# Kernel optimization log

Measured on AMD Instinct MI355X. Metric: run time of the kernel, lower is better.

The kernel has to match this reference:

```python
import jax, jax.numpy as jnp
import numpy as np
import math

B, T, EMB, HEAD = 4, 4096, 768, 64


def setup_inputs() -> dict:
    key = jax.random.key(0)
    kx, kk, kq, kv = jax.random.split(key, 4)
    s = 1.0 / math.sqrt(EMB)  # roughly torch Linear init scale
    return {
        "x": jax.random.normal(kx, (B, T, EMB), dtype=jnp.float32),
        "Wk": jax.random.normal(kk, (EMB, HEAD), dtype=jnp.float32) * s,
        "Wq": jax.random.normal(kq, (EMB, HEAD), dtype=jnp.float32) * s,
        "Wv": jax.random.normal(kv, (EMB, HEAD), dtype=jnp.float32) * s,
    }


def reference(x, Wk, Wq, Wv):
    # x: (B, T, EMB); projections are bias-free Linear layers
    k = x @ Wk  # (B, T, HEAD)
    q = x @ Wq
    v = x @ Wv
    Tcur = x.shape[1]
    scale = 1.0 / math.sqrt(k.shape[-1])
    # (B, Tq, Tk) score matrix, causal masked
    wei = jnp.einsum("bqh,bkh->bqk", q, k) * scale
    causal = jnp.tril(jnp.ones((Tcur, Tcur), dtype=bool))
    wei = jnp.where(causal, wei, -jnp.inf)
    attn = jax.nn.softmax(wei, axis=-1)  # dropout p=0.0 (eval)
    return jnp.einsum("bqk,bkh->bqh", attn, v)  # (B, T, HEAD)
```

## Files before the change

kernel.cpp:

```cpp
#include <hip/hip_runtime.h>
#include <hip/hip_bf16.h>

#define NB 4
#define NT 4096
#define NE 768
#define NH 64

using bf16 = __hip_bfloat16;
typedef __attribute__((ext_vector_type(8))) short bf16x8;
typedef __attribute__((ext_vector_type(4))) float f32x4;
typedef __attribute__((ext_vector_type(16))) float f32x16;
typedef __attribute__((ext_vector_type(4))) unsigned int u32x4;

#define QSCALE 0.18033688011112042f

__device__ inline short f2bfs(float f) {
  bf16 h = __float2bfloat16(f);
  return __builtin_bit_cast(short, h);
}
__device__ inline unsigned pack_bf2(float a, float b) {
  unsigned short ua = __builtin_bit_cast(unsigned short, __float2bfloat16(a));
  unsigned short ub = __builtin_bit_cast(unsigned short, __float2bfloat16(b));
  return ((unsigned)ub << 16) | ua;
}

#define GLOAD_LDS16(gsrc, ldst)                                        \
  __builtin_amdgcn_global_load_lds(                                    \
      (const __attribute__((address_space(1))) void*)(gsrc),           \
      (__attribute__((address_space(3))) void*)(ldst), 16, 0, 0)

__global__ __launch_bounds__(256) void k_wt(const float* __restrict__ Wk,
                                            const float* __restrict__ Wq,
                                            const float* __restrict__ Wv,
                                            bf16* __restrict__ Wt2) {
  __shared__ float xl[32][65];
  const int m = blockIdx.x / 24;
  const int ks = blockIdx.x % 24;
  const int tid = threadIdx.x;
  const float* W = (m == 0) ? Wk : ((m == 1) ? Wq : Wv);
  const float scale = (m == 1) ? QSCALE : 1.0f;
  const int e0 = ks * 32;
#pragma unroll
  for (int i = 0; i < 8; ++i) {
    const int lin = i * 256 + tid;
    xl[lin >> 6][lin & 63] = W[(size_t)(e0 + (lin >> 6)) * NH + (lin & 63)];
  }
  __syncthreads();
  const int lane = tid & 63, w = tid >> 6;
  const int cbg = m * 4 + w;
  bf16x8 t;
#pragma unroll
  for (int j = 0; j < 8; ++j)
    t[j] = f2bfs(xl[((lane >> 4) << 3) + j][w * 16 + (lane & 15)] * scale);
  *reinterpret_cast<bf16x8*>(Wt2 + (((size_t)cbg * 24 + ks) * 64 + lane) * 8) = t;
}

__global__ __launch_bounds__(256) void k_proj(const float* __restrict__ x,
                                              const bf16* __restrict__ Wt2,
                                              bf16* __restrict__ Q,
                                              bf16* __restrict__ K,
                                              bf16* __restrict__ Vt) {
  __shared__ __align__(16) bf16 xl[16][768];
  const int tid = threadIdx.x;
  const int wave = tid >> 6, lane = tid & 63;
  const int lr = lane & 15, lk = lane >> 4;
  const int row0 = blockIdx.x * 16;

#pragma unroll
  for (int j = 0; j < 6; ++j) {
    const int e = (j * 256 + tid) * 8;
    const int row = e / 768;
    const int col = e - row * 768;
    const int chunk = col >> 3;
    const int sch = (chunk & ~7) | ((chunk ^ row) & 7);
    const float* xp = x + (size_t)(row0 + row) * NE + col;
    float4 a0 = *reinterpret_cast<const float4*>(xp);
    float4 a1 = *reinterpret_cast<const float4*>(xp + 4);
    bf16x8 af;
    af[0] = f2bfs(a0.x); af[1] = f2bfs(a0.y); af[2] = f2bfs(a0.z); af[3] = f2bfs(a0.w);
    af[4] = f2bfs(a1.x); af[5] = f2bfs(a1.y); af[6] = f2bfs(a1.z); af[7] = f2bfs(a1.w);
    *reinterpret_cast<bf16x8*>((char*)xl + row * 1536 + sch * 16) = af;
  }
  __syncthreads();

  f32x4 acc[3];
#pragma unroll
  for (int cb = 0; cb < 3; ++cb)
#pragma unroll
    for (int r = 0; r < 4; ++r) acc[cb][r] = 0.f;

#pragma unroll 4
  for (int ks = 0; ks < 24; ++ks) {
    const int chunk = ks * 4 + lk;
    const int sch = (chunk & ~7) | ((chunk ^ lr) & 7);
    bf16x8 af = *reinterpret_cast<const bf16x8*>((const char*)xl + lr * 1536 + sch * 16);
#pragma unroll
    for (int cb = 0; cb < 3; ++cb) {
      bf16x8 bfr = *reinterpret_cast<const bf16x8*>(
          Wt2 + (((size_t)(wave * 3 + cb) * 24 + ks) * 64 + lane) * 8);
      acc[cb] = __builtin_amdgcn_mfma_f32_16x16x32_bf16(af, bfr, acc[cb], 0, 0, 0);
    }
  }

  const int trow = row0 + lk * 4;
#pragma unroll
  for (int cb = 0; cb < 3; ++cb) {
    const int hh0 = (wave * 3 + cb) * 16;
    const int m = hh0 >> 6;
    const int h = (hh0 & 63) + lr;
    if (m == 0) {
#pragma unroll
      for (int r = 0; r < 4; ++r)
        K[(size_t)(trow + r) * NH + h] = __float2bfloat16(acc[cb][r]);
    } else if (m == 1) {
#pragma unroll
      for (int r = 0; r < 4; ++r)
        Q[(size_t)(trow + r) * NH + h] = __float2bfloat16(acc[cb][r]);
    } else {
      const int bb = trow >> 12;
      const int t = trow & (NT - 1);
      ushort4 pk;
      pk.x = (unsigned short)f2bfs(acc[cb][0]);
      pk.y = (unsigned short)f2bfs(acc[cb][1]);
      pk.z = (unsigned short)f2bfs(acc[cb][2]);
      pk.w = (unsigned short)f2bfs(acc[cb][3]);
      *reinterpret_cast<ushort4*>(Vt + (size_t)(bb * NH + h) * NT + t) = pk;
    }
  }
}

__device__ inline void stage_kv(const bf16* Kb, const bf16* Vb, int k0,
                                bf16* Kl, bf16* Vl, int wave, int lane) {
  const int rsub = lane >> 3, ch = lane & 7;
#pragma unroll
  for (int j = 0; j < 2; ++j) {
    const int br = j * 32 + wave * 8;
    const int row = br + rsub;
    const int sch = ch ^ (row & 7);
    GLOAD_LDS16(Kb + (size_t)(k0 + row) * NH + sch * 8, Kl + br * 64);
    GLOAD_LDS16(Vb + (size_t)row * NT + k0 + sch * 8, Vl + br * 64);
  }
}

__global__ __launch_bounds__(256) void k_attn_part(const bf16* __restrict__ Q,
                                                   const bf16* __restrict__ K,
                                                   const bf16* __restrict__ Vt,
                                                   float* __restrict__ part_o,
                                                   float* __restrict__ part_ml,
                                                   int CH, int MAXC) {
  __shared__ __align__(16) bf16 Kl[2][64][64];
  __shared__ __align__(16) bf16 Vl[2][64][64];
  const int tid = threadIdx.x;
  const int wave = tid >> 6, lane = tid & 63;
  const int l31 = lane & 31, hi5 = lane >> 5;
  const int gid = blockIdx.x;
  const int c = gid % MAXC;
  const int srs = (gid / MAXC) & 31;
  const int b = gid / (MAXC * 32);
  const int s = 31 - srs;
  const int ntiles = 2 * s + 2;
  const int nch = (ntiles + CH - 1) / CH;
  if (c >= nch) return;
  const int kt0 = c * CH;
  const int kt1 = min(kt0 + CH, ntiles);
  const int qblk = s * 128;
  const int qrow = 8 * wave + (l31 & 7) + 32 * (l31 >> 3);
  const int qcol = qblk + qrow;

  const bf16* Qb = Q + (size_t)(b * NT + qcol) * NH;
  const bf16* Kb = K + (size_t)b * NT * NH;
  const bf16* Vb = Vt + (size_t)b * NH * NT;

  bf16x8 qf[4];
#pragma unroll
  for (int ks = 0; ks < 4; ++ks)
    qf[ks] = *reinterpret_cast<const bf16x8*>(Qb + ks * 16 + hi5 * 8);

  f32x16 o[2];
#pragma unroll
  for (int hb = 0; hb < 2; ++hb)
#pragma unroll
    for (int r = 0; r < 16; ++r) o[hb][r] = 0.f;
  float m = -1e30f, lsum = 0.f;

  stage_kv(Kb, Vb, kt0 * 64, &Kl[0][0][0], &Vl[0][0][0], wave, lane);

  for (int kt = kt0; kt < kt1; ++kt) {
    const int buf = (kt - kt0) & 1;
    __syncthreads();
    if (kt + 1 < kt1)
      stage_kv(Kb, Vb, (kt + 1) * 64, &Kl[buf ^ 1][0][0], &Vl[buf ^ 1][0][0], wave, lane);
    const int k0 = kt * 64;
    const bf16* Klb = &Kl[buf][0][0];
    const bf16* Vlb = &Vl[buf][0][0];

    f32x16 sa[2];
#pragma unroll
    for (int kb = 0; kb < 2; ++kb) {
#pragma unroll
      for (int r = 0; r < 16; ++r) sa[kb][r] = 0.f;
      __builtin_amdgcn_s_setprio(1);
#pragma unroll
      for (int ks = 0; ks < 4; ++ks) {
        const int row = l31 + 32 * kb;
        const int sch = (hi5 + 2 * ks) ^ (row & 7);
        bf16x8 kf = *reinterpret_cast<const bf16x8*>(Klb + row * 64 + sch * 8);
        sa[kb] = __builtin_amdgcn_mfma_f32_32x32x16_bf16(kf, qf[ks], sa[kb], 0, 0, 0);
      }
      __builtin_amdgcn_s_setprio(0);
    }
    if (kt >= 2 * s) {
#pragma unroll
      for (int kb = 0; kb < 2; ++kb)
#pragma unroll
        for (int r = 0; r < 16; ++r) {
          const int kg = k0 + (r & 3) + 8 * (r >> 2) + 4 * hi5 + 32 * kb;
          if (kg > qcol) sa[kb][r] = -1e30f;
        }
    }
    float pm = sa[0][0];
#pragma unroll
    for (int r = 1; r < 16; ++r) pm = fmaxf(pm, sa[0][r]);
#pragma unroll
    for (int r = 0; r < 16; ++r) pm = fmaxf(pm, sa[1][r]);
    pm = fmaxf(pm, __shfl_xor(pm, 32));
    if (!__all(pm - m <= 6.f)) {
      const float mn = fmaxf(m, pm);
      const float alpha = exp2f(m - mn);
      lsum *= alpha;
#pragma unroll
      for (int hb = 0; hb < 2; ++hb)
#pragma unroll
        for (int r = 0; r < 16; ++r) o[hb][r] *= alpha;
      m = mn;
    }
    float rs = 0.f;
#pragma unroll
    for (int kb = 0; kb < 2; ++kb)
#pragma unroll
      for (int r = 0; r < 16; ++r) {
        const float p = exp2f(sa[kb][r] - m);
        sa[kb][r] = p;
        rs += p;
      }
    rs += __shfl_xor(rs, 32);
    lsum += rs;
    unsigned pk[2][4][2];
#pragma unroll
    for (int kb = 0; kb < 2; ++kb)
#pragma unroll
      for (int q4 = 0; q4 < 4; ++q4)
#pragma unroll
        for (int p = 0; p < 2; ++p)
          pk[kb][q4][p] = pack_bf2(sa[kb][4 * q4 + 2 * p], sa[kb][4 * q4 + 2 * p + 1]);
#pragma unroll
    for (int kb16 = 0; kb16 < 4; ++kb16) {
      const int kb32 = kb16 >> 1;
      const int q4a = 2 * (kb16 & 1);
      const unsigned X0 = pk[kb32][q4a][0], X1 = pk[kb32][q4a][1];
      const unsigned Y0 = pk[kb32][q4a + 1][0], Y1 = pk[kb32][q4a + 1][1];
      const unsigned pX0 = __shfl_xor((int)X0, 32), pX1 = __shfl_xor((int)X1, 32);
      const unsigned pY0 = __shfl_xor((int)Y0, 32), pY1 = __shfl_xor((int)Y1, 32);
      u32x4 pw;
      pw[0] = hi5 ? pY0 : X0;
      pw[1] = hi5 ? pY1 : X1;
      pw[2] = hi5 ? Y0 : pX0;
      pw[3] = hi5 ? Y1 : pX1;
      const bf16x8 pf = __builtin_bit_cast(bf16x8, pw);
      __builtin_amdgcn_s_setprio(1);
#pragma unroll
      for (int hb = 0; hb < 2; ++hb) {
        const int row = l31 + 32 * hb;
        const int sch = (hi5 + 2 * kb16) ^ (row & 7);
        bf16x8 vf = *reinterpret_cast<const bf16x8*>(Vlb + row * 64 + sch * 8);
        o[hb] = __builtin_amdgcn_mfma_f32_32x32x16_bf16(vf, pf, o[hb], 0, 0, 0);
      }
      __builtin_amdgcn_s_setprio(0);
    }
  }

  const size_t idx = (size_t)(b * 32 + s) * MAXC + c;
  float* po = part_o + idx * (128 * 64);
#pragma unroll
  for (int hb = 0; hb < 2; ++hb)
#pragma unroll
    for (int q4 = 0; q4 < 4; ++q4) {
      const int h0 = 32 * hb + 8 * q4 + 4 * hi5;
      float4 v;
      v.x = o[hb][4 * q4 + 0];
      v.y = o[hb][4 * q4 + 1];
      v.z = o[hb][4 * q4 + 2];
      v.w = o[hb][4 * q4 + 3];
      *reinterpret_cast<float4*>(po + (size_t)qrow * 64 + h0) = v;
    }
  if (hi5 == 0) {
    float* pml = part_ml + idx * 256;
    pml[qrow] = m;
    pml[128 + qrow] = lsum;
  }
}

__global__ __launch_bounds__(256) void k_attn_comb(const float* __restrict__ part_o,
                                                   const float* __restrict__ part_ml,
                                                   float* __restrict__ out,
                                                   int CH, int MAXC) {
  const int gid = blockIdx.x;
  const int s = gid & 31;
  const int b = gid >> 5;
  const int row = threadIdx.x >> 1;
  const int half = threadIdx.x & 1;
  const int ntiles = 2 * s + 2;
  const int nc = (ntiles + CH - 1) / CH;
  const size_t base = (size_t)(b * 32 + s) * MAXC;

  float M = -1e30f;
  for (int c = 0; c < nc; ++c)
    M = fmaxf(M, part_ml[(base + c) * 256 + row]);
  float L = 0.f;
  float4 a[8];
#pragma unroll
  for (int k = 0; k < 8; ++k) a[k] = float4{0, 0, 0, 0};
  for (int c = 0; c < nc; ++c) {
    const float mc = part_ml[(base + c) * 256 + row];
    const float lc = part_ml[(base + c) * 256 + 128 + row];
    const float sc = exp2f(mc - M);
    L += lc * sc;
    const float4* op = reinterpret_cast<const float4*>(
        part_o + (base + c) * (128 * 64) + (size_t)row * 64 + half * 32);
#pragma unroll
    for (int k = 0; k < 8; ++k) {
      const float4 v = op[k];
      a[k].x += v.x * sc; a[k].y += v.y * sc;
      a[k].z += v.z * sc; a[k].w += v.w * sc;
    }
  }
  const float inv = 1.f / L;
  float4* outp = reinterpret_cast<float4*>(
      out + (size_t)(b * NT + s * 128 + row) * NH + half * 32);
#pragma unroll
  for (int k = 0; k < 8; ++k) {
    a[k].x *= inv; a[k].y *= inv; a[k].z *= inv; a[k].w *= inv;
    outp[k] = a[k];
  }
}

extern "C" void kernel_launch(void* const* d_in, const int* in_sizes, int n_in,
                              void* d_out, int out_size, void* d_ws, size_t ws_size,
                              hipStream_t stream) {
  const float* x  = (const float*)d_in[0];
  const float* Wk = (const float*)d_in[1];
  const float* Wq = (const float*)d_in[2];
  const float* Wv = (const float*)d_in[3];
  float* out = (float*)d_out;

  char* ws = (char*)d_ws;
  const size_t sz_wt  = (size_t)3 * NH * NE * sizeof(bf16);
  const size_t sz_qkv = (size_t)NB * NT * NH * sizeof(bf16);
  const size_t off_q  = (sz_wt + 255) & ~size_t(255);
  const size_t off_k  = off_q + sz_qkv;
  const size_t off_vt = off_k + sz_qkv;
  const size_t off_pp = off_vt + sz_qkv;

  const size_t per_chunk = (size_t)(128 * 64 + 256) * sizeof(float);
  int CH = 64, MAXC = 1;
  const int opts_ch[3]   = {6, 8, 16};
  const int opts_maxc[3] = {11, 8, 4};
  for (int i = 0; i < 3; ++i) {
    const size_t need = off_pp + (size_t)NB * 32 * opts_maxc[i] * per_chunk;
    if (ws_size >= need) { CH = opts_ch[i]; MAXC = opts_maxc[i]; break; }
  }
  const size_t n_idx = (size_t)NB * 32 * MAXC;
  const size_t off_po = off_pp;
  const size_t off_ml = off_po + n_idx * (128 * 64) * sizeof(float);

  bf16* Wt2 = (bf16*)(ws);
  bf16* Qw  = (bf16*)(ws + off_q);
  bf16* Kw  = (bf16*)(ws + off_k);
  bf16* Vtw = (bf16*)(ws + off_vt);
  float* part_o  = (float*)(ws + off_po);
  float* part_ml = (float*)(ws + off_ml);

  hipLaunchKernelGGL(k_wt, dim3(3 * 24), dim3(256), 0, stream, Wk, Wq, Wv, Wt2);
  hipLaunchKernelGGL(k_proj, dim3(NB * NT / 16), dim3(256), 0, stream,
                     x, Wt2, Qw, Kw, Vtw);
  hipLaunchKernelGGL(k_attn_part, dim3(NB * 32 * MAXC), dim3(256), 0, stream,
                     Qw, Kw, Vtw, part_o, part_ml, CH, MAXC);
  hipLaunchKernelGGL(k_attn_comb, dim3(NB * 32), dim3(256), 0, stream,
                     part_o, part_ml, out, CH, MAXC);
}
```

Measured before the change: 157.3 us.

## Restructure attention into per-wave query blocks and split x conversion out

Attention now gives each wave its own 32-query unit and reads K/V fragments straight from global memory into registers, dropping the LDS double buffer and block-wide syncs. Partial outputs are stored as bf16 and the combine kernel is re-indexed to match the smaller query blocks. x is converted to bf16 in a separate prep kernel fused with the weight transpose. The projection kernel keeps weight fragments in registers and uses a grid split by Q/K/V. This trades extra global traffic and register pressure for finer load balance and no LDS synchronisation, and lowers the precision of the partial outputs.

```diff
diff --git a/kernel.cpp b/kernel.cpp
--- a/kernel.cpp
+++ b/kernel.cpp
@@ -18,6 +18,10 @@
   bf16 h = __float2bfloat16(f);
   return __builtin_bit_cast(short, h);
 }
+__device__ inline float bfs2f(unsigned short u) {
+  unsigned v = ((unsigned)u) << 16;
+  return __builtin_bit_cast(float, v);
+}
 __device__ inline unsigned pack_bf2(float a, float b) {
   unsigned short ua = __builtin_bit_cast(unsigned short, __float2bfloat16(a));
   unsigned short ub = __builtin_bit_cast(unsigned short, __float2bfloat16(b));
@@ -29,143 +33,135 @@
       (const __attribute__((address_space(1))) void*)(gsrc),           \
       (__attribute__((address_space(3))) void*)(ldst), 16, 0, 0)
 
-__global__ __launch_bounds__(256) void k_wt(const float* __restrict__ Wk,
-                                            const float* __restrict__ Wq,
-                                            const float* __restrict__ Wv,
-                                            bf16* __restrict__ Wt2) {
-  __shared__ float xl[32][65];
-  const int m = blockIdx.x / 24;
-  const int ks = blockIdx.x % 24;
+__global__ __launch_bounds__(256) void k_prep(const float* __restrict__ x,
+                                              const float* __restrict__ Wk,
+                                              const float* __restrict__ Wq,
+                                              const float* __restrict__ Wv,
+                                              bf16* __restrict__ Wt2,
+                                              bf16* __restrict__ xb) {
+  __shared__ float wl[32][65];
   const int tid = threadIdx.x;
-  const float* W = (m == 0) ? Wk : ((m == 1) ? Wq : Wv);
-  const float scale = (m == 1) ? QSCALE : 1.0f;
-  const int e0 = ks * 32;
-#pragma unroll
-  for (int i = 0; i < 8; ++i) {
-    const int lin = i * 256 + tid;
-    xl[lin >> 6][lin & 63] = W[(size_t)(e0 + (lin >> 6)) * NH + (lin & 63)];
-  }
-  __syncthreads();
-  const int lane = tid & 63, w = tid >> 6;
-  const int cbg = m * 4 + w;
-  bf16x8 t;
-#pragma unroll
-  for (int j = 0; j < 8; ++j)
-    t[j] = f2bfs(xl[((lane >> 4) << 3) + j][w * 16 + (lane & 15)] * scale);
-  *reinterpret_cast<bf16x8*>(Wt2 + (((size_t)cbg * 24 + ks) * 64 + lane) * 8) = t;
-}
-
-__global__ __launch_bounds__(256) void k_proj(const float* __restrict__ x,
+  if (blockIdx.x < 72) {
+    const int m = blockIdx.x / 24;
+    const int ks = blockIdx.x % 24;
+    const float* W = (m == 0) ? Wk : ((m == 1) ? Wq : Wv);
+    const float scale = (m == 1) ? QSCALE : 1.0f;
+#pragma unroll
+    for (int i = 0; i < 8; ++i) {
+      const int lin = i * 256 + tid;
+      wl[lin >> 6][lin & 63] = W[(size_t)(ks * 32 + (lin >> 6)) * NH + (lin & 63)];
+    }
+    __syncthreads();
+    const int lane = tid & 63, w = tid >> 6;
+    const int cbg = m * 4 + w;
+    bf16x8 t;
+#pragma unroll
+    for (int j = 0; j < 8; ++j)
+      t[j] = f2bfs(wl[((lane >> 4) << 3) + j][w * 16 + (lane & 15)] * scale);
+    *reinterpret_cast<bf16x8*>(Wt2 + (((size_t)cbg * 24 + ks) * 64 + lane) * 8) = t;
+    return;
+  }
+  const size_t e0 = ((size_t)(blockIdx.x - 72) * 256 + tid) * 8;
+  const int row = (int)(e0 / 768);
+  const int col = (int)(e0 - (size_t)row * 768);
+  const int chunk = col >> 3;
+  const int sch = (chunk & ~7) | ((chunk ^ row) & 7);
+  float4 a0 = *reinterpret_cast<const float4*>(x + e0);
+  float4 a1 = *reinterpret_cast<const float4*>(x + e0 + 4);
+  bf16x8 af;
+  af[0] = f2bfs(a0.x); af[1] = f2bfs(a0.y); af[2] = f2bfs(a0.z); af[3] = f2bfs(a0.w);
+  af[4] = f2bfs(a1.x); af[5] = f2bfs(a1.y); af[6] = f2bfs(a1.z); af[7] = f2bfs(a1.w);
+  *reinterpret_cast<bf16x8*>(xb + (size_t)row * 768 + sch * 8) = af;
+}
+
+__global__ __launch_bounds__(256) void k_proj(const bf16* __restrict__ xb,
                                               const bf16* __restrict__ Wt2,
                                               bf16* __restrict__ Q,
                                               bf16* __restrict__ K,
                                               bf16* __restrict__ Vt) {
-  __shared__ __align__(16) bf16 xl[16][768];
+  __shared__ __align__(16) bf16 xl[32][768];
   const int tid = threadIdx.x;
   const int wave = tid >> 6, lane = tid & 63;
   const int lr = lane & 15, lk = lane >> 4;
-  const int row0 = blockIdx.x * 16;
-
-#pragma unroll
-  for (int j = 0; j < 6; ++j) {
-    const int e = (j * 256 + tid) * 8;
-    const int row = e / 768;
-    const int col = e - row * 768;
-    const int chunk = col >> 3;
-    const int sch = (chunk & ~7) | ((chunk ^ row) & 7);
-    const float* xp = x + (size_t)(row0 + row) * NE + col;
-    float4 a0 = *reinterpret_cast<const float4*>(xp);
-    float4 a1 = *reinterpret_cast<const float4*>(xp + 4);
-    bf16x8 af;
-    af[0] = f2bfs(a0.x); af[1] = f2bfs(a0.y); af[2] = f2bfs(a0.z); af[3] = f2bfs(a0.w);
-    af[4] = f2bfs(a1.x); af[5] = f2bfs(a1.y); af[6] = f2bfs(a1.z); af[7] = f2bfs(a1.w);
-    *reinterpret_cast<bf16x8*>((char*)xl + row * 1536 + sch * 16) = af;
-  }
-  __syncthreads();
-
-  f32x4 acc[3];
-#pragma unroll
-  for (int cb = 0; cb < 3; ++cb)
-#pragma unroll
-    for (int r = 0; r < 4; ++r) acc[cb][r] = 0.f;
-
-#pragma unroll 4
-  for (int ks = 0; ks < 24; ++ks) {
-    const int chunk = ks * 4 + lk;
-    const int sch = (chunk & ~7) | ((chunk ^ lr) & 7);
-    bf16x8 af = *reinterpret_cast<const bf16x8*>((const char*)xl + lr * 1536 + sch * 16);
-#pragma unroll
-    for (int cb = 0; cb < 3; ++cb) {
-      bf16x8 bfr = *reinterpret_cast<const bf16x8*>(
-          Wt2 + (((size_t)(wave * 3 + cb) * 24 + ks) * 64 + lane) * 8);
-      acc[cb] = __builtin_amdgcn_mfma_f32_16x16x32_bf16(af, bfr, acc[cb], 0, 0, 0);
-    }
-  }
-
-  const int trow = row0 + lk * 4;
-#pragma unroll
-  for (int cb = 0; cb < 3; ++cb) {
-    const int hh0 = (wave * 3 + cb) * 16;
-    const int m = hh0 >> 6;
-    const int h = (hh0 & 63) + lr;
-    if (m == 0) {
-#pragma unroll
-      for (int r = 0; r < 4; ++r)
-        K[(size_t)(trow + r) * NH + h] = __float2bfloat16(acc[cb][r]);
-    } else if (m == 1) {
-#pragma unroll
-      for (int r = 0; r < 4; ++r)
-        Q[(size_t)(trow + r) * NH + h] = __float2bfloat16(acc[cb][r]);
-    } else {
-      const int bb = trow >> 12;
-      const int t = trow & (NT - 1);
-      ushort4 pk;
-      pk.x = (unsigned short)f2bfs(acc[cb][0]);
-      pk.y = (unsigned short)f2bfs(acc[cb][1]);
-      pk.z = (unsigned short)f2bfs(acc[cb][2]);
-      pk.w = (unsigned short)f2bfs(acc[cb][3]);
-      *reinterpret_cast<ushort4*>(Vt + (size_t)(bb * NH + h) * NT + t) = pk;
-    }
-  }
-}
-
-__device__ inline void stage_kv(const bf16* Kb, const bf16* Vb, int k0,
-                                bf16* Kl, bf16* Vl, int wave, int lane) {
-  const int rsub = lane >> 3, ch = lane & 7;
-#pragma unroll
-  for (int j = 0; j < 2; ++j) {
-    const int br = j * 32 + wave * 8;
-    const int row = br + rsub;
-    const int sch = ch ^ (row & 7);
-    GLOAD_LDS16(Kb + (size_t)(k0 + row) * NH + sch * 8, Kl + br * 64);
-    GLOAD_LDS16(Vb + (size_t)row * NT + k0 + sch * 8, Vl + br * 64);
+  const int m = blockIdx.y;
+  const int cbg = m * 4 + wave;
+
+  bf16x8 wf[24];
+#pragma unroll
+  for (int ks = 0; ks < 24; ++ks)
+    wf[ks] = *reinterpret_cast<const bf16x8*>(
+        Wt2 + (((size_t)cbg * 24 + ks) * 64 + lane) * 8);
+
+  for (int grp = 0; grp < 2; ++grp) {
+    const int t0 = blockIdx.x * 64 + grp * 32;
+#pragma unroll
+    for (int i = 0; i < 12; ++i)
+      GLOAD_LDS16(xb + (size_t)t0 * 768 + ((size_t)i * 256 + tid) * 8,
+                  (char*)xl + (i * 256 + tid) * 16);
+    __syncthreads();
+
+    f32x4 a0, a1;
+#pragma unroll
+    for (int r = 0; r < 4; ++r) { a0[r] = 0.f; a1[r] = 0.f; }
+#pragma unroll
+    for (int ks = 0; ks < 24; ++ks) {
+      const int chunk = ks * 4 + lk;
+      const int sch = (chunk & ~7) | ((chunk ^ lr) & 7);
+      bf16x8 af0 = *reinterpret_cast<const bf16x8*>((const char*)xl + lr * 1536 + sch * 16);
+      bf16x8 af1 = *reinterpret_cast<const bf16x8*>((const char*)xl + (16 + lr) * 1536 + sch * 16);
+      a0 = __builtin_amdgcn_mfma_f32_16x16x32_bf16(af0, wf[ks], a0, 0, 0, 0);
+      a1 = __builtin_amdgcn_mfma_f32_16x16x32_bf16(af1, wf[ks], a1, 0, 0, 0);
+    }
+
+#pragma unroll
+    for (int sub = 0; sub < 2; ++sub) {
+      const f32x4 a = sub ? a1 : a0;
+      const int trow = t0 + sub * 16 + lk * 4;
+      const int h = wave * 16 + lr;
+      if (m == 0) {
+#pragma unroll
+        for (int r = 0; r < 4; ++r)
+          K[(size_t)(trow + r) * NH + h] = __float2bfloat16(a[r]);
+      } else if (m == 1) {
+#pragma unroll
+        for (int r = 0; r < 4; ++r)
+          Q[(size_t)(trow + r) * NH + h] = __float2bfloat16(a[r]);
+      } else {
+        const int bb = trow >> 12;
+        const int t = trow & (NT - 1);
+        ushort4 pk4;
+        pk4.x = (unsigned short)f2bfs(a[0]);
+        pk4.y = (unsigned short)f2bfs(a[1]);
+        pk4.z = (unsigned short)f2bfs(a[2]);
+        pk4.w = (unsigned short)f2bfs(a[3]);
+        *reinterpret_cast<ushort4*>(Vt + (size_t)(bb * NH + h) * NT + t) = pk4;
+      }
+    }
+    __syncthreads();
   }
 }
 
 __global__ __launch_bounds__(256) void k_attn_part(const bf16* __restrict__ Q,
                                                    const bf16* __restrict__ K,
                                                    const bf16* __restrict__ Vt,
-                                                   float* __restrict__ part_o,
+                                                   bf16* __restrict__ part_o,
                                                    float* __restrict__ part_ml,
                                                    int CH, int MAXC) {
-  __shared__ __align__(16) bf16 Kl[2][64][64];
-  __shared__ __align__(16) bf16 Vl[2][64][64];
   const int tid = threadIdx.x;
   const int wave = tid >> 6, lane = tid & 63;
   const int l31 = lane & 31, hi5 = lane >> 5;
-  const int gid = blockIdx.x;
-  const int c = gid % MAXC;
-  const int srs = (gid / MAXC) & 31;
-  const int b = gid / (MAXC * 32);
-  const int s = 31 - srs;
-  const int ntiles = 2 * s + 2;
+  const int unit = blockIdx.x * 4 + wave;
+  const int c = unit % MAXC;
+  const int srs = (unit / MAXC) & 127;
+  const int b = unit / (MAXC * 128);
+  const int s = 127 - srs;
+  const int ntiles = (s >> 1) + 1;
   const int nch = (ntiles + CH - 1) / CH;
   if (c >= nch) return;
-  const int kt0 = c * CH;
-  const int kt1 = min(kt0 + CH, ntiles);
-  const int qblk = s * 128;
-  const int qrow = 8 * wave + (l31 & 7) + 32 * (l31 >> 3);
-  const int qcol = qblk + qrow;
+  const int kt0c = c * CH;
+  const int ktend = min(kt0c + CH, ntiles);
+  const int qblk = s * 32;
+  const int qcol = qblk + l31;
 
   const bf16* Qb = Q + (size_t)(b * NT + qcol) * NH;
   const bf16* Kb = K + (size_t)b * NT * NH;
@@ -183,16 +179,22 @@
     for (int r = 0; r < 16; ++r) o[hb][r] = 0.f;
   float m = -1e30f, lsum = 0.f;
 
-  stage_kv(Kb, Vb, kt0 * 64, &Kl[0][0][0], &Vl[0][0][0], wave, lane);
-
-  for (int kt = kt0; kt < kt1; ++kt) {
-    const int buf = (kt - kt0) & 1;
-    __syncthreads();
-    if (kt + 1 < kt1)
-      stage_kv(Kb, Vb, (kt + 1) * 64, &Kl[buf ^ 1][0][0], &Vl[buf ^ 1][0][0], wave, lane);
+  for (int kt = kt0c; kt < ktend; ++kt) {
     const int k0 = kt * 64;
-    const bf16* Klb = &Kl[buf][0][0];
-    const bf16* Vlb = &Vl[buf][0][0];
+    bf16x8 kf[2][4];
+#pragma unroll
+    for (int kb = 0; kb < 2; ++kb)
+#pragma unroll
+      for (int ks = 0; ks < 4; ++ks)
+        kf[kb][ks] = *reinterpret_cast<const bf16x8*>(
+            Kb + (size_t)(k0 + 32 * kb + l31) * NH + ks * 16 + hi5 * 8);
+    bf16x8 vf[4][2];
+#pragma unroll
+    for (int kb16 = 0; kb16 < 4; ++kb16)
+#pragma unroll
+      for (int hb = 0; hb < 2; ++hb)
+        vf[kb16][hb] = *reinterpret_cast<const bf16x8*>(
+            Vb + (size_t)(l31 + 32 * hb) * NT + k0 + kb16 * 16 + hi5 * 8);
 
     f32x16 sa[2];
 #pragma unroll
@@ -201,15 +203,11 @@
       for (int r = 0; r < 16; ++r) sa[kb][r] = 0.f;
       __builtin_amdgcn_s_setprio(1);
 #pragma unroll
-      for (int ks = 0; ks < 4; ++ks) {
-        const int row = l31 + 32 * kb;
-        const int sch = (hi5 + 2 * ks) ^ (row & 7);
-        bf16x8 kf = *reinterpret_cast<const bf16x8*>(Klb + row * 64 + sch * 8);
-        sa[kb] = __builtin_amdgcn_mfma_f32_32x32x16_bf16(kf, qf[ks], sa[kb], 0, 0, 0);
-      }
+      for (int ks = 0; ks < 4; ++ks)
+        sa[kb] = __builtin_amdgcn_mfma_f32_32x32x16_bf16(kf[kb][ks], qf[ks], sa[kb], 0, 0, 0);
       __builtin_amdgcn_s_setprio(0);
     }
-    if (kt >= 2 * s) {
+    if (kt == ntiles - 1) {
 #pragma unroll
       for (int kb = 0; kb < 2; ++kb)
 #pragma unroll
@@ -218,11 +216,12 @@
           if (kg > qcol) sa[kb][r] = -1e30f;
         }
     }
-    float pm = sa[0][0];
-#pragma unroll
-    for (int r = 1; r < 16; ++r) pm = fmaxf(pm, sa[0][r]);
-#pragma unroll
-    for (int r = 0; r < 16; ++r) pm = fmaxf(pm, sa[1][r]);
+    float t0[8];
+#pragma unroll
+    for (int r = 0; r < 8; ++r)
+      t0[r] = fmaxf(fmaxf(sa[0][r], sa[0][r + 8]), fmaxf(sa[1][r], sa[1][r + 8]));
+    float pm = fmaxf(fmaxf(fmaxf(t0[0], t0[1]), fmaxf(t0[2], t0[3])),
+                     fmaxf(fmaxf(t0[4], t0[5]), fmaxf(t0[6], t0[7])));
     pm = fmaxf(pm, __shfl_xor(pm, 32));
     if (!__all(pm - m <= 6.f)) {
       const float mn = fmaxf(m, pm);
@@ -234,15 +233,17 @@
         for (int r = 0; r < 16; ++r) o[hb][r] *= alpha;
       m = mn;
     }
-    float rs = 0.f;
+    float rs0 = 0.f, rs1 = 0.f, rs2 = 0.f, rs3 = 0.f;
 #pragma unroll
     for (int kb = 0; kb < 2; ++kb)
 #pragma unroll
-      for (int r = 0; r < 16; ++r) {
-        const float p = exp2f(sa[kb][r] - m);
-        sa[kb][r] = p;
-        rs += p;
+      for (int r = 0; r < 16; r += 4) {
+        sa[kb][r] = exp2f(sa[kb][r] - m); rs0 += sa[kb][r];
+        sa[kb][r + 1] = exp2f(sa[kb][r + 1] - m); rs1 += sa[kb][r + 1];
+        sa[kb][r + 2] = exp2f(sa[kb][r + 2] - m); rs2 += sa[kb][r + 2];
+        sa[kb][r + 3] = exp2f(sa[kb][r + 3] - m); rs3 += sa[kb][r + 3];
       }
+    float rs = (rs0 + rs1) + (rs2 + rs3);
     rs += __shfl_xor(rs, 32);
     lsum += rs;
     unsigned pk[2][4][2];
@@ -269,79 +270,68 @@
       const bf16x8 pf = __builtin_bit_cast(bf16x8, pw);
       __builtin_amdgcn_s_setprio(1);
 #pragma unroll
-      for (int hb = 0; hb < 2; ++hb) {
-        const int row = l31 + 32 * hb;
-        const int sch = (hi5 + 2 * kb16) ^ (row & 7);
-        bf16x8 vf = *reinterpret_cast<const bf16x8*>(Vlb + row * 64 + sch * 8);
-        o[hb] = __builtin_amdgcn_mfma_f32_32x32x16_bf16(vf, pf, o[hb], 0, 0, 0);
-      }
+      for (int hb = 0; hb < 2; ++hb)
+        o[hb] = __builtin_amdgcn_mfma_f32_32x32x16_bf16(vf[kb16][hb], pf, o[hb], 0, 0, 0);
       __builtin_amdgcn_s_setprio(0);
     }
   }
 
-  const size_t idx = (size_t)(b * 32 + s) * MAXC + c;
-  float* po = part_o + idx * (128 * 64);
+  const size_t idx = (size_t)(b * 128 + s) * MAXC + c;
+  bf16* po = part_o + idx * (32 * 64);
 #pragma unroll
   for (int hb = 0; hb < 2; ++hb)
 #pragma unroll
     for (int q4 = 0; q4 < 4; ++q4) {
       const int h0 = 32 * hb + 8 * q4 + 4 * hi5;
-      float4 v;
-      v.x = o[hb][4 * q4 + 0];
-      v.y = o[hb][4 * q4 + 1];
-      v.z = o[hb][4 * q4 + 2];
-      v.w = o[hb][4 * q4 + 3];
-      *reinterpret_cast<float4*>(po + (size_t)qrow * 64 + h0) = v;
+      ushort4 pk4;
+      pk4.x = (unsigned short)f2bfs(o[hb][4 * q4 + 0]);
+      pk4.y = (unsigned short)f2bfs(o[hb][4 * q4 + 1]);
+      pk4.z = (unsigned short)f2bfs(o[hb][4 * q4 + 2]);
+      pk4.w = (unsigned short)f2bfs(o[hb][4 * q4 + 3]);
+      *reinterpret_cast<ushort4*>(po + (size_t)l31 * 64 + h0) = pk4;
     }
   if (hi5 == 0) {
-    float* pml = part_ml + idx * 256;
-    pml[qrow] = m;
-    pml[128 + qrow] = lsum;
-  }
-}
-
-__global__ __launch_bounds__(256) void k_attn_comb(const float* __restrict__ part_o,
+    float* pml = part_ml + idx * 64;
+    pml[l31] = m;
+    pml[32 + l31] = lsum;
+  }
+}
+
+__global__ __launch_bounds__(256) void k_attn_comb(const bf16* __restrict__ part_o,
                                                    const float* __restrict__ part_ml,
                                                    float* __restrict__ out,
                                                    int CH, int MAXC) {
   const int gid = blockIdx.x;
-  const int s = gid & 31;
-  const int b = gid >> 5;
-  const int row = threadIdx.x >> 1;
-  const int half = threadIdx.x & 1;
-  const int ntiles = 2 * s + 2;
+  const int rg = gid & 1;
+  const int s = (gid >> 1) & 127;
+  const int b = gid >> 8;
+  const int row = rg * 16 + (threadIdx.x >> 4);
+  const int cq = threadIdx.x & 15;
+  const int ntiles = (s >> 1) + 1;
   const int nc = (ntiles + CH - 1) / CH;
-  const size_t base = (size_t)(b * 32 + s) * MAXC;
+  const size_t base = (size_t)(b * 128 + s) * MAXC;
 
   float M = -1e30f;
   for (int c = 0; c < nc; ++c)
-    M = fmaxf(M, part_ml[(base + c) * 256 + row]);
-  float L = 0.f;
-  float4 a[8];
-#pragma unroll
-  for (int k = 0; k < 8; ++k) a[k] = float4{0, 0, 0, 0};
+    M = fmaxf(M, part_ml[(base + c) * 64 + row]);
+  float L = 0.f, a0 = 0.f, a1 = 0.f, a2 = 0.f, a3 = 0.f;
   for (int c = 0; c < nc; ++c) {
-    const float mc = part_ml[(base + c) * 256 + row];
-    const float lc = part_ml[(base + c) * 256 + 128 + row];
+    const float mc = part_ml[(base + c) * 64 + row];
+    const float lc = part_ml[(base + c) * 64 + 32 + row];
     const float sc = exp2f(mc - M);
     L += lc * sc;
-    const float4* op = reinterpret_cast<const float4*>(
-        part_o + (base + c) * (128 * 64) + (size_t)row * 64 + half * 32);
-#pragma unroll
-    for (int k = 0; k < 8; ++k) {
-      const float4 v = op[k];
-      a[k].x += v.x * sc; a[k].y += v.y * sc;
-      a[k].z += v.z * sc; a[k].w += v.w * sc;
-    }
+    ushort4 v = *reinterpret_cast<const ushort4*>(
+        part_o + (base + c) * (32 * 64) + (size_t)row * 64 + cq * 4);
+    a0 += bfs2f(v.x) * sc;
+    a1 += bfs2f(v.y) * sc;
+    a2 += bfs2f(v.z) * sc;
+    a3 += bfs2f(v.w) * sc;
   }
   const float inv = 1.f / L;
-  float4* outp = reinterpret_cast<float4*>(
-      out + (size_t)(b * NT + s * 128 + row) * NH + half * 32);
-#pragma unroll
-  for (int k = 0; k < 8; ++k) {
-    a[k].x *= inv; a[k].y *= inv; a[k].z *= inv; a[k].w *= inv;
-    outp[k] = a[k];
-  }
+  float4 ov;
+  ov.x = a0 * inv; ov.y = a1 * inv; ov.z = a2 * inv; ov.w = a3 * inv;
+  *reinterpret_cast<float4*>(
+      out + (size_t)(b * NT + s * 32 + row) * NH + cq * 4) = ov;
 }
 
 extern "C" void kernel_launch(void* const* d_in, const int* in_sizes, int n_in,
@@ -354,37 +344,41 @@
   float* out = (float*)d_out;
 
   char* ws = (char*)d_ws;
-  const size_t sz_wt  = (size_t)3 * NH * NE * sizeof(bf16);
+  const size_t sz_wt  = (size_t)12 * 24 * 64 * 8 * sizeof(bf16);
+  const size_t sz_xb  = (size_t)NB * NT * NE * sizeof(bf16);
   const size_t sz_qkv = (size_t)NB * NT * NH * sizeof(bf16);
-  const size_t off_q  = (sz_wt + 255) & ~size_t(255);
+  const size_t off_xb = (sz_wt + 255) & ~size_t(255);
+  const size_t off_q  = off_xb + sz_xb;
   const size_t off_k  = off_q + sz_qkv;
   const size_t off_vt = off_k + sz_qkv;
   const size_t off_pp = off_vt + sz_qkv;
 
-  const size_t per_chunk = (size_t)(128 * 64 + 256) * sizeof(float);
   int CH = 64, MAXC = 1;
-  const int opts_ch[3]   = {6, 8, 16};
-  const int opts_maxc[3] = {11, 8, 4};
-  for (int i = 0; i < 3; ++i) {
-    const size_t need = off_pp + (size_t)NB * 32 * opts_maxc[i] * per_chunk;
+  const int opts_ch[4]   = {4, 8, 16, 64};
+  const int opts_maxc[4] = {16, 8, 4, 1};
+  for (int i = 0; i < 4; ++i) {
+    const size_t n_idx = (size_t)NB * 128 * opts_maxc[i];
+    const size_t need = off_pp + n_idx * (4096 + 256);
     if (ws_size >= need) { CH = opts_ch[i]; MAXC = opts_maxc[i]; break; }
   }
-  const size_t n_idx = (size_t)NB * 32 * MAXC;
+  const size_t n_idx = (size_t)NB * 128 * MAXC;
   const size_t off_po = off_pp;
-  const size_t off_ml = off_po + n_idx * (128 * 64) * sizeof(float);
+  const size_t off_ml = off_po + n_idx * 4096;
 
   bf16* Wt2 = (bf16*)(ws);
+  bf16* xb  = (bf16*)(ws + off_xb);
   bf16* Qw  = (bf16*)(ws + off_q);
   bf16* Kw  = (bf16*)(ws + off_k);
   bf16* Vtw = (bf16*)(ws + off_vt);
-  float* part_o  = (float*)(ws + off_po);
+  bf16* part_o   = (bf16*)(ws + off_po);
   float* part_ml = (float*)(ws + off_ml);
 
-  hipLaunchKernelGGL(k_wt, dim3(3 * 24), dim3(256), 0, stream, Wk, Wq, Wv, Wt2);
-  hipLaunchKernelGGL(k_proj, dim3(NB * NT / 16), dim3(256), 0, stream,
-                     x, Wt2, Qw, Kw, Vtw);
-  hipLaunchKernelGGL(k_attn_part, dim3(NB * 32 * MAXC), dim3(256), 0, stream,
+  hipLaunchKernelGGL(k_prep, dim3(72 + NB * NT * NE / 2048), dim3(256), 0, stream,
+                     x, Wk, Wq, Wv, Wt2, xb);
+  hipLaunchKernelGGL(k_proj, dim3(NB * NT / 64, 3), dim3(256), 0, stream,
+                     xb, Wt2, Qw, Kw, Vtw);
+  hipLaunchKernelGGL(k_attn_part, dim3(NB * 128 * MAXC / 4), dim3(256), 0, stream,
                      Qw, Kw, Vtw, part_o, part_ml, CH, MAXC);
-  hipLaunchKernelGGL(k_attn_comb, dim3(NB * 32), dim3(256), 0, stream,
+  hipLaunchKernelGGL(k_attn_comb, dim3(NB * 128 * 2), dim3(256), 0, stream,
                      part_o, part_ml, out, CH, MAXC);
 }
```

Measured after the change: 179.0 us. 13.8% more time.

## Store bf16 partials, retile projection, widen combine grid, drop setprio, tree reductions

Applied to the files above, without the earlier changes.

The projection kernel now processes 32 rows per block, so each W fragment loaded from global memory feeds two MFMAs. Attention partial outputs are stored as bf16 with nontemporal stores, which halves partial traffic, and the split-K chunk size drops to 4 tiles when the workspace allows. The combine kernel runs eight times as many blocks, with each thread handling four columns. The setprio hints are removed, and the max and sum reductions are split into independent chains for ILP. Rounding the partials to bf16 costs some precision in the final output.

```diff
diff --git a/kernel.cpp b/kernel.cpp
--- a/kernel.cpp
+++ b/kernel.cpp
@@ -18,10 +18,18 @@
   bf16 h = __float2bfloat16(f);
   return __builtin_bit_cast(short, h);
 }
+__device__ inline float bfs2f(unsigned short u) {
+  unsigned v = ((unsigned)u) << 16;
+  return __builtin_bit_cast(float, v);
+}
 __device__ inline unsigned pack_bf2(float a, float b) {
   unsigned short ua = __builtin_bit_cast(unsigned short, __float2bfloat16(a));
   unsigned short ub = __builtin_bit_cast(unsigned short, __float2bfloat16(b));
   return ((unsigned)ub << 16) | ua;
+}
+__device__ inline void nt_store8(void* p, ushort4 v) {
+  __builtin_nontemporal_store(__builtin_bit_cast(unsigned long long, v),
+                              (unsigned long long*)p);
 }
 
 #define GLOAD_LDS16(gsrc, ldst)                                        \
@@ -60,14 +68,14 @@
                                               bf16* __restrict__ Q,
                                               bf16* __restrict__ K,
                                               bf16* __restrict__ Vt) {
-  __shared__ __align__(16) bf16 xl[16][768];
+  __shared__ __align__(16) bf16 xl[32][768];
   const int tid = threadIdx.x;
   const int wave = tid >> 6, lane = tid & 63;
   const int lr = lane & 15, lk = lane >> 4;
-  const int row0 = blockIdx.x * 16;
-
-#pragma unroll
-  for (int j = 0; j < 6; ++j) {
+  const int row0 = blockIdx.x * 32;
+
+#pragma unroll
+  for (int j = 0; j < 12; ++j) {
     const int e = (j * 256 + tid) * 8;
     const int row = e / 768;
     const int col = e - row * 768;
@@ -83,48 +91,54 @@
   }
   __syncthreads();
 
-  f32x4 acc[3];
+  f32x4 acc0[3], acc1[3];
 #pragma unroll
   for (int cb = 0; cb < 3; ++cb)
 #pragma unroll
-    for (int r = 0; r < 4; ++r) acc[cb][r] = 0.f;
+    for (int r = 0; r < 4; ++r) { acc0[cb][r] = 0.f; acc1[cb][r] = 0.f; }
 
 #pragma unroll 4
   for (int ks = 0; ks < 24; ++ks) {
     const int chunk = ks * 4 + lk;
     const int sch = (chunk & ~7) | ((chunk ^ lr) & 7);
-    bf16x8 af = *reinterpret_cast<const bf16x8*>((const char*)xl + lr * 1536 + sch * 16);
+    bf16x8 af0 = *reinterpret_cast<const bf16x8*>((const char*)xl + lr * 1536 + sch * 16);
+    bf16x8 af1 = *reinterpret_cast<const bf16x8*>((const char*)xl + (16 + lr) * 1536 + sch * 16);
 #pragma unroll
     for (int cb = 0; cb < 3; ++cb) {
       bf16x8 bfr = *reinterpret_cast<const bf16x8*>(
           Wt2 + (((size_t)(wave * 3 + cb) * 24 + ks) * 64 + lane) * 8);
-      acc[cb] = __builtin_amdgcn_mfma_f32_16x16x32_bf16(af, bfr, acc[cb], 0, 0, 0);
-    }
-  }
-
-  const int trow = row0 + lk * 4;
-#pragma unroll
-  for (int cb = 0; cb < 3; ++cb) {
-    const int hh0 = (wave * 3 + cb) * 16;
-    const int m = hh0 >> 6;
-    const int h = (hh0 & 63) + lr;
-    if (m == 0) {
-#pragma unroll
-      for (int r = 0; r < 4; ++r)
-        K[(size_t)(trow + r) * NH + h] = __float2bfloat16(acc[cb][r]);
-    } else if (m == 1) {
-#pragma unroll
-      for (int r = 0; r < 4; ++r)
-        Q[(size_t)(trow + r) * NH + h] = __float2bfloat16(acc[cb][r]);
-    } else {
-      const int bb = trow >> 12;
-      const int t = trow & (NT - 1);
-      ushort4 pk;
-      pk.x = (unsigned short)f2bfs(acc[cb][0]);
-      pk.y = (unsigned short)f2bfs(acc[cb][1]);
-      pk.z = (unsigned short)f2bfs(acc[cb][2]);
-      pk.w = (unsigned short)f2bfs(acc[cb][3]);
-      *reinterpret_cast<ushort4*>(Vt + (size_t)(bb * NH + h) * NT + t) = pk;
+      acc0[cb] = __builtin_amdgcn_mfma_f32_16x16x32_bf16(af0, bfr, acc0[cb], 0, 0, 0);
+      acc1[cb] = __builtin_amdgcn_mfma_f32_16x16x32_bf16(af1, bfr, acc1[cb], 0, 0, 0);
+    }
+  }
+
+#pragma unroll
+  for (int st = 0; st < 2; ++st) {
+    const int trow = row0 + st * 16 + lk * 4;
+#pragma unroll
+    for (int cb = 0; cb < 3; ++cb) {
+      const f32x4 a = st ? acc1[cb] : acc0[cb];
+      const int hh0 = (wave * 3 + cb) * 16;
+      const int m = hh0 >> 6;
+      const int h = (hh0 & 63) + lr;
+      if (m == 0) {
+#pragma unroll
+        for (int r = 0; r < 4; ++r)
+          K[(size_t)(trow + r) * NH + h] = __float2bfloat16(a[r]);
+      } else if (m == 1) {
+#pragma unroll
+        for (int r = 0; r < 4; ++r)
+          Q[(size_t)(trow + r) * NH + h] = __float2bfloat16(a[r]);
+      } else {
+        const int bb = trow >> 12;
+        const int t = trow & (NT - 1);
+        ushort4 pk4;
+        pk4.x = (unsigned short)f2bfs(a[0]);
+        pk4.y = (unsigned short)f2bfs(a[1]);
+        pk4.z = (unsigned short)f2bfs(a[2]);
+        pk4.w = (unsigned short)f2bfs(a[3]);
+        *reinterpret_cast<ushort4*>(Vt + (size_t)(bb * NH + h) * NT + t) = pk4;
+      }
     }
   }
 }
@@ -145,7 +159,7 @@
 __global__ __launch_bounds__(256) void k_attn_part(const bf16* __restrict__ Q,
                                                    const bf16* __restrict__ K,
                                                    const bf16* __restrict__ Vt,
-                                                   float* __restrict__ part_o,
+                                                   bf16* __restrict__ part_o,
                                                    float* __restrict__ part_ml,
                                                    int CH, int MAXC) {
   __shared__ __align__(16) bf16 Kl[2][64][64];
@@ -199,7 +213,6 @@
     for (int kb = 0; kb < 2; ++kb) {
 #pragma unroll
       for (int r = 0; r < 16; ++r) sa[kb][r] = 0.f;
-      __builtin_amdgcn_s_setprio(1);
 #pragma unroll
       for (int ks = 0; ks < 4; ++ks) {
         const int row = l31 + 32 * kb;
@@ -207,7 +220,6 @@
         bf16x8 kf = *reinterpret_cast<const bf16x8*>(Klb + row * 64 + sch * 8);
         sa[kb] = __builtin_amdgcn_mfma_f32_32x32x16_bf16(kf, qf[ks], sa[kb], 0, 0, 0);
       }
-      __builtin_amdgcn_s_setprio(0);
     }
     if (kt >= 2 * s) {
 #pragma unroll
@@ -218,11 +230,12 @@
           if (kg > qcol) sa[kb][r] = -1e30f;
         }
     }
-    float pm = sa[0][0];
-#pragma unroll
-    for (int r = 1; r < 16; ++r) pm = fmaxf(pm, sa[0][r]);
-#pragma unroll
-    for (int r = 0; r < 16; ++r) pm = fmaxf(pm, sa[1][r]);
+    float t0[8];
+#pragma unroll
+    for (int r = 0; r < 8; ++r)
+      t0[r] = fmaxf(fmaxf(sa[0][r], sa[0][r + 8]), fmaxf(sa[1][r], sa[1][r + 8]));
+    float pm = fmaxf(fmaxf(fmaxf(t0[0], t0[1]), fmaxf(t0[2], t0[3])),
+                     fmaxf(fmaxf(t0[4], t0[5]), fmaxf(t0[6], t0[7])));
     pm = fmaxf(pm, __shfl_xor(pm, 32));
     if (!__all(pm - m <= 6.f)) {
       const float mn = fmaxf(m, pm);
@@ -234,15 +247,17 @@
         for (int r = 0; r < 16; ++r) o[hb][r] *= alpha;
       m = mn;
     }
-    float rs = 0.f;
+    float rs0 = 0.f, rs1 = 0.f, rs2 = 0.f, rs3 = 0.f;
 #pragma unroll
     for (int kb = 0; kb < 2; ++kb)
 #pragma unroll
-      for (int r = 0; r < 16; ++r) {
-        const float p = exp2f(sa[kb][r] - m);
-        sa[kb][r] = p;
-        rs += p;
+      for (int r = 0; r < 16; r += 4) {
+        sa[kb][r] = exp2f(sa[kb][r] - m); rs0 += sa[kb][r];
+        sa[kb][r + 1] = exp2f(sa[kb][r + 1] - m); rs1 += sa[kb][r + 1];
+        sa[kb][r + 2] = exp2f(sa[kb][r + 2] - m); rs2 += sa[kb][r + 2];
+        sa[kb][r + 3] = exp2f(sa[kb][r + 3] - m); rs3 += sa[kb][r + 3];
       }
+    float rs = (rs0 + rs1) + (rs2 + rs3);
     rs += __shfl_xor(rs, 32);
     lsum += rs;
     unsigned pk[2][4][2];
@@ -267,7 +282,6 @@
       pw[2] = hi5 ? Y0 : pX0;
       pw[3] = hi5 ? Y1 : pX1;
       const bf16x8 pf = __builtin_bit_cast(bf16x8, pw);
-      __builtin_amdgcn_s_setprio(1);
 #pragma unroll
       for (int hb = 0; hb < 2; ++hb) {
         const int row = l31 + 32 * hb;
@@ -275,23 +289,22 @@
         bf16x8 vf = *reinterpret_cast<const bf16x8*>(Vlb + row * 64 + sch * 8);
         o[hb] = __builtin_amdgcn_mfma_f32_32x32x16_bf16(vf, pf, o[hb], 0, 0, 0);
       }
-      __builtin_amdgcn_s_setprio(0);
     }
   }
 
   const size_t idx = (size_t)(b * 32 + s) * MAXC + c;
-  float* po = part_o + idx * (128 * 64);
+  bf16* po = part_o + idx * (128 * 64);
 #pragma unroll
   for (int hb = 0; hb < 2; ++hb)
 #pragma unroll
     for (int q4 = 0; q4 < 4; ++q4) {
       const int h0 = 32 * hb + 8 * q4 + 4 * hi5;
-      float4 v;
-      v.x = o[hb][4 * q4 + 0];
-      v.y = o[hb][4 * q4 + 1];
-      v.z = o[hb][4 * q4 + 2];
-      v.w = o[hb][4 * q4 + 3];
-      *reinterpret_cast<float4*>(po + (size_t)qrow * 64 + h0) = v;
+      ushort4 pk4;
+      pk4.x = (unsigned short)f2bfs(o[hb][4 * q4 + 0]);
+      pk4.y = (unsigned short)f2bfs(o[hb][4 * q4 + 1]);
+      pk4.z = (unsigned short)f2bfs(o[hb][4 * q4 + 2]);
+      pk4.w = (unsigned short)f2bfs(o[hb][4 * q4 + 3]);
+      nt_store8(po + (size_t)qrow * 64 + h0, pk4);
     }
   if (hi5 == 0) {
     float* pml = part_ml + idx * 256;
@@ -300,15 +313,16 @@
   }
 }
 
-__global__ __launch_bounds__(256) void k_attn_comb(const float* __restrict__ part_o,
+__global__ __launch_bounds__(256) void k_attn_comb(const bf16* __restrict__ part_o,
                                                    const float* __restrict__ part_ml,
                                                    float* __restrict__ out,
                                                    int CH, int MAXC) {
   const int gid = blockIdx.x;
-  const int s = gid & 31;
-  const int b = gid >> 5;
-  const int row = threadIdx.x >> 1;
-  const int half = threadIdx.x & 1;
+  const int rg = gid & 7;
+  const int s = (gid >> 3) & 31;
+  const int b = gid >> 8;
+  const int row = rg * 16 + (threadIdx.x >> 4);
+  const int cq = threadIdx.x & 15;
   const int ntiles = 2 * s + 2;
   const int nc = (ntiles + CH - 1) / CH;
   const size_t base = (size_t)(b * 32 + s) * MAXC;
@@ -316,32 +330,24 @@
   float M = -1e30f;
   for (int c = 0; c < nc; ++c)
     M = fmaxf(M, part_ml[(base + c) * 256 + row]);
-  float L = 0.f;
-  float4 a[8];
-#pragma unroll
-  for (int k = 0; k < 8; ++k) a[k] = float4{0, 0, 0, 0};
+  float L = 0.f, a0 = 0.f, a1 = 0.f, a2 = 0.f, a3 = 0.f;
   for (int c = 0; c < nc; ++c) {
     const float mc = part_ml[(base + c) * 256 + row];
     const float lc = part_ml[(base + c) * 256 + 128 + row];
     const float sc = exp2f(mc - M);
     L += lc * sc;
-    const float4* op = reinterpret_cast<const float4*>(
-        part_o + (base + c) * (128 * 64) + (size_t)row * 64 + half * 32);
-#pragma unroll
-    for (int k = 0; k < 8; ++k) {
-      const float4 v = op[k];
-      a[k].x += v.x * sc; a[k].y += v.y * sc;
-      a[k].z += v.z * sc; a[k].w += v.w * sc;
-    }
+    ushort4 v = *reinterpret_cast<const ushort4*>(
+        part_o + (base + c) * (128 * 64) + (size_t)row * 64 + cq * 4);
+    a0 += bfs2f(v.x) * sc;
+    a1 += bfs2f(v.y) * sc;
+    a2 += bfs2f(v.z) * sc;
+    a3 += bfs2f(v.w) * sc;
   }
   const float inv = 1.f / L;
-  float4* outp = reinterpret_cast<float4*>(
-      out + (size_t)(b * NT + s * 128 + row) * NH + half * 32);
-#pragma unroll
-  for (int k = 0; k < 8; ++k) {
-    a[k].x *= inv; a[k].y *= inv; a[k].z *= inv; a[k].w *= inv;
-    outp[k] = a[k];
-  }
+  float4 ov;
+  ov.x = a0 * inv; ov.y = a1 * inv; ov.z = a2 * inv; ov.w = a3 * inv;
+  *reinterpret_cast<float4*>(
+      out + (size_t)(b * NT + s * 128 + row) * NH + cq * 4) = ov;
 }
 
 extern "C" void kernel_launch(void* const* d_in, const int* in_sizes, int n_in,
@@ -354,37 +360,37 @@
   float* out = (float*)d_out;
 
   char* ws = (char*)d_ws;
-  const size_t sz_wt  = (size_t)3 * NH * NE * sizeof(bf16);
+  const size_t sz_wt  = (size_t)12 * 24 * 64 * 8 * sizeof(bf16);
   const size_t sz_qkv = (size_t)NB * NT * NH * sizeof(bf16);
   const size_t off_q  = (sz_wt + 255) & ~size_t(255);
   const size_t off_k  = off_q + sz_qkv;
   const size_t off_vt = off_k + sz_qkv;
   const size_t off_pp = off_vt + sz_qkv;
 
-  const size_t per_chunk = (size_t)(128 * 64 + 256) * sizeof(float);
+  const size_t per_chunk = (size_t)128 * 64 * sizeof(bf16) + 256 * sizeof(float);
   int CH = 64, MAXC = 1;
-  const int opts_ch[3]   = {6, 8, 16};
-  const int opts_maxc[3] = {11, 8, 4};
-  for (int i = 0; i < 3; ++i) {
+  const int opts_ch[4]   = {4, 6, 8, 16};
+  const int opts_maxc[4] = {16, 11, 8, 4};
+  for (int i = 0; i < 4; ++i) {
     const size_t need = off_pp + (size_t)NB * 32 * opts_maxc[i] * per_chunk;
     if (ws_size >= need) { CH = opts_ch[i]; MAXC = opts_maxc[i]; break; }
   }
   const size_t n_idx = (size_t)NB * 32 * MAXC;
   const size_t off_po = off_pp;
-  const size_t off_ml = off_po + n_idx * (128 * 64) * sizeof(float);
+  const size_t off_ml = off_po + n_idx * (size_t)(128 * 64) * sizeof(bf16);
 
   bf16* Wt2 = (bf16*)(ws);
   bf16* Qw  = (bf16*)(ws + off_q);
   bf16* Kw  = (bf16*)(ws + off_k);
   bf16* Vtw = (bf16*)(ws + off_vt);
-  float* part_o  = (float*)(ws + off_po);
+  bf16* part_o   = (bf16*)(ws + off_po);
   float* part_ml = (float*)(ws + off_ml);
 
   hipLaunchKernelGGL(k_wt, dim3(3 * 24), dim3(256), 0, stream, Wk, Wq, Wv, Wt2);
-  hipLaunchKernelGGL(k_proj, dim3(NB * NT / 16), dim3(256), 0, stream,
+  hipLaunchKernelGGL(k_proj, dim3(NB * NT / 32), dim3(256), 0, stream,
                      x, Wt2, Qw, Kw, Vtw);
   hipLaunchKernelGGL(k_attn_part, dim3(NB * 32 * MAXC), dim3(256), 0, stream,
                      Qw, Kw, Vtw, part_o, part_ml, CH, MAXC);
-  hipLaunchKernelGGL(k_attn_comb, dim3(NB * 32), dim3(256), 0, stream,
+  hipLaunchKernelGGL(k_attn_comb, dim3(NB * 32 * 8), dim3(256), 0, stream,
                      part_o, part_ml, out, CH, MAXC);
 }
```

New measurement: 162.1 us. +3.0%, slower.
